# Kernel tuning notes

Measured on AMD Instinct MI355X. Metric: run time of the kernel, lower is better.

Reference implementation:

```python
import jax, jax.numpy as jnp
import numpy as np

B, SQ, SK, D, H = 2, 2048, 2048, 1024, 16
DK = D // H


def setup_inputs() -> dict:
    key = jax.random.key(0)
    ks = jax.random.split(key, 16)
    s = 1.0 / np.sqrt(D)
    inp = {
        "query": jax.random.normal(ks[0], (B, SQ, D), jnp.float32),
        "key": jax.random.normal(ks[1], (B, SK, D), jnp.float32),
        "value": jax.random.normal(ks[2], (B, SK, D), jnp.float32),
        "R": jax.random.normal(ks[3], (B, SK, D), jnp.float32),
        "Wq": jax.random.normal(ks[4], (D, D), jnp.float32) * s,
        "bq": jnp.zeros((D,), jnp.float32),
        "Wv": jax.random.normal(ks[5], (D, D), jnp.float32) * s,
        "bv": jnp.zeros((D,), jnp.float32),
        "Wr": jax.random.normal(ks[6], (D, D), jnp.float32) * s,
        "br": jnp.zeros((D,), jnp.float32),
        "W_h": jax.random.normal(ks[7], (H, DK, DK), jnp.float32) * (1.0 / np.sqrt(DK)),
        "Wo": jax.random.normal(ks[8], (D, D), jnp.float32) * s,
        "bo": jnp.zeros((D,), jnp.float32),
    }
    return inp


def _forward(query, key, value, R, Wq, bq, Wv, bv, Wr, br, W_h, Wo, bo):
    scale = 1.0 / np.sqrt(DK)
    # projections (torch Linear: x @ W.T + b)
    Q = (query @ Wq.T + bq).reshape(B, SQ, H, DK).transpose(0, 2, 1, 3)   # (B,H,SQ,DK)
    V = (value @ Wv.T + bv).reshape(B, SK, H, DK).transpose(0, 2, 1, 3)   # (B,H,SK,DK)
    Rp = (R @ Wr.T + br).reshape(B, SK, H, DK).transpose(0, 2, 1, 3)      # (B,H,SK,DK)
    # torch einsum 'hnk,bhn->bhn' sums W_h over its last axis -> elementwise gate
    w_rowsum = W_h.sum(axis=-1)  # (H, DK)

    def step(h, r_t):
        h_new = jnp.tanh(h * w_rowsum + r_t)  # (B,H,DK)
        return h_new, h_new

    h0 = jnp.zeros((B, H, DK), Rp.dtype)
    Rt = Rp.transpose(2, 0, 1, 3)  # (SK,B,H,DK)
    _, Hs = jax.lax.scan(step, h0, Rt)
    Hst = Hs.transpose(1, 2, 0, 3)  # (B,H,SK,DK)

    scores = jnp.einsum('bhqd,bhkd->bhqk', Q, Hst) * scale
    attn = jax.nn.softmax(scores, axis=-1)
    out = jnp.einsum('bhqk,bhkd->bhqd', attn, V)
    out = out.transpose(0, 2, 1, 3).reshape(B, SQ, D)
    return out @ Wo.T + bo


def reference(query, key, value, R, Wq, bq, Wv, bv, Wr, br, W_h, Wo, bo):
    return _forward(query, key, value, R, Wq, bq, Wv, bv, Wr, br, W_h, Wo, bo)
```

## Files before the change

kernel.cpp:

```cpp
#include <hip/hip_runtime.h>
#include <stdint.h>

typedef unsigned short u16;
typedef __attribute__((ext_vector_type(8))) _Float16 h8;
typedef __attribute__((ext_vector_type(2))) __fp16 hp2;
typedef __attribute__((ext_vector_type(4))) float f4;

#define B_ 2
#define SQ_ 2048
#define SK_ 2048
#define D_ 1024
#define H_ 16
#define DK_ 64

__device__ __forceinline__ u16 f2h(float f) {
  union { _Float16 h; u16 u; } v; v.h = (_Float16)f; return v.u;
}
__device__ __forceinline__ float h2f(u16 b) {
  union { u16 u; _Float16 h; } v; v.u = b; return (float)v.h;
}
__device__ __forceinline__ unsigned pkrtz(float a, float b) {
  union { hp2 h; unsigned u; } v; v.h = __builtin_amdgcn_cvt_pkrtz(a, b); return v.u;
}
__device__ __forceinline__ float fexp2(float x) {
  float r;
  asm("v_exp_f32 %0, %1" : "=v"(r) : "v"(x));
  return r;
}

typedef const void __attribute__((address_space(1)))* gas1;
typedef void __attribute__((address_space(3)))* las3;
__device__ __forceinline__ void gld16(const void* g, void* l) {
  __builtin_amdgcn_global_load_lds((gas1)g, (las3)l, 16, 0, 0);
}

__global__ void rma_cast(const float* __restrict__ xq, const float* __restrict__ xv,
                         const float* __restrict__ xr, const float* __restrict__ w0,
                         const float* __restrict__ w1, const float* __restrict__ w2,
                         const float* __restrict__ w3, u16* __restrict__ oq,
                         u16* __restrict__ ov, u16* __restrict__ orr,
                         u16* __restrict__ o0, u16* __restrict__ o1,
                         u16* __restrict__ o2, u16* __restrict__ o3) {
  const int z = blockIdx.z;
  if (z >= 3 && blockIdx.x >= 512) return;
  const float* src;
  u16* dst;
  switch (z) {
    case 0: src = xq; dst = oq; break;
    case 1: src = xv; dst = ov; break;
    case 2: src = xr; dst = orr; break;
    case 3: src = w0; dst = o0; break;
    case 4: src = w1; dst = o1; break;
    case 5: src = w2; dst = o2; break;
    default: src = w3; dst = o3; break;
  }
  int i = (blockIdx.x * 256 + threadIdx.x) * 8;
  float4 a = *(const float4*)(src + i);
  float4 b = *(const float4*)(src + i + 4);
  alignas(16) u16 t[8] = {f2h(a.x), f2h(a.y), f2h(a.z), f2h(a.w),
                          f2h(b.x), f2h(b.y), f2h(b.z), f2h(b.w)};
  *(int4*)(dst + i) = *(int4*)t;
}

__device__ __forceinline__ void gemm_mainloop(
    const u16* __restrict__ A, const u16* __restrict__ Bw, int K,
    u16* As, u16* Bs, int m0, int n0, f4 (&acc)[4][4]) {
  const int tid = threadIdx.x;
  const int w = tid >> 6, lane = tid & 63;
  const int quad = lane >> 4, ln = lane & 15;
  const int wm = (w >> 1) * 64, wn = (w & 1) * 64;
  const int c0 = tid, c1 = tid + 256;
  const u16* a0 = A + (size_t)(m0 + (c0 >> 2)) * K + (c0 & 3) * 8;
  const u16* a1 = A + (size_t)(m0 + (c1 >> 2)) * K + (c1 & 3) * 8;
  const u16* b0 = Bw + (size_t)(n0 + (c0 >> 2)) * K + (c0 & 3) * 8;
  const u16* b1 = Bw + (size_t)(n0 + (c1 >> 2)) * K + (c1 & 3) * 8;
  u16* As0 = As + (0 + w * 64) * 8;
  u16* As1 = As + (256 + w * 64) * 8;
  u16* Bs0 = Bs + (0 + w * 64) * 8;
  u16* Bs1 = Bs + (256 + w * 64) * 8;
  for (int kt = 0; kt < K; kt += 32) {
    gld16(a0 + kt, As0);
    gld16(a1 + kt, As1);
    gld16(b0 + kt, Bs0);
    gld16(b1 + kt, Bs1);
    __syncthreads();
    h8 af[4], bf[4];
#pragma unroll
    for (int i = 0; i < 4; i++)
      af[i] = *(const h8*)&As[(wm + i * 16 + ln) * 32 + quad * 8];
#pragma unroll
    for (int i = 0; i < 4; i++)
      bf[i] = *(const h8*)&Bs[(wn + i * 16 + ln) * 32 + quad * 8];
#pragma unroll
    for (int i = 0; i < 4; i++)
#pragma unroll
      for (int j = 0; j < 4; j++)
        acc[i][j] = __builtin_amdgcn_mfma_f32_16x16x32_f16(af[i], bf[j], acc[i][j], 0, 0, 0);
    __syncthreads();
  }
}

__device__ __forceinline__ void gemm_mainloop64(
    const u16* __restrict__ A, const u16* __restrict__ Bw, int K,
    u16* As, u16* Bs, int m0, int n0, f4 (&acc)[2][4]) {
  const int tid = threadIdx.x;
  const int w = tid >> 6, lane = tid & 63;
  const int quad = lane >> 4, ln = lane & 15;
  const int wm = (w >> 1) * 32, wn = (w & 1) * 64;
  const u16* a0 = A + (size_t)(m0 + (tid >> 2)) * K + (tid & 3) * 8;
  const u16* b0 = Bw + (size_t)(n0 + (tid >> 2)) * K + (tid & 3) * 8;
  const u16* b1 = Bw + (size_t)(n0 + ((tid + 256) >> 2)) * K + (tid & 3) * 8;
  u16* As0 = As + (w * 64) * 8;
  u16* Bs0 = Bs + (w * 64) * 8;
  u16* Bs1 = Bs + (256 + w * 64) * 8;
  for (int kt = 0; kt < K; kt += 32) {
    gld16(a0 + kt, As0);
    gld16(b0 + kt, Bs0);
    gld16(b1 + kt, Bs1);
    __syncthreads();
    h8 af[2], bf[4];
#pragma unroll
    for (int i = 0; i < 2; i++)
      af[i] = *(const h8*)&As[(wm + i * 16 + ln) * 32 + quad * 8];
#pragma unroll
    for (int j = 0; j < 4; j++)
      bf[j] = *(const h8*)&Bs[(wn + j * 16 + ln) * 32 + quad * 8];
#pragma unroll
    for (int i = 0; i < 2; i++)
#pragma unroll
      for (int j = 0; j < 4; j++)
        acc[i][j] = __builtin_amdgcn_mfma_f32_16x16x32_f16(af[i], bf[j], acc[i][j], 0, 0, 0);
    __syncthreads();
  }
}

__global__ __launch_bounds__(256, 2)
void rma_proj_gemm(const u16* __restrict__ Xq, const u16* __restrict__ Xv,
                   const u16* __restrict__ Xr, const u16* __restrict__ Wq,
                   const u16* __restrict__ Wv, const u16* __restrict__ Wr,
                   const float* __restrict__ bq, const float* __restrict__ bv,
                   const float* __restrict__ br, u16* __restrict__ Qb,
                   u16* __restrict__ Vt, float* __restrict__ Rp) {
  const int z = blockIdx.z;
  const u16* A = z == 0 ? Xq : (z == 1 ? Xv : Xr);
  const u16* Bw = z == 0 ? Wq : (z == 1 ? Wv : Wr);
  const float* bias = z == 0 ? bq : (z == 1 ? bv : br);
  __shared__ u16 As[128 * 32];
  __shared__ u16 Bs[128 * 32];
  const int m0 = blockIdx.x * 128, n0 = blockIdx.y * 128;
  f4 acc[4][4] = {};
  gemm_mainloop(A, Bw, D_, As, Bs, m0, n0, acc);
  const int tid = threadIdx.x;
  const int w = tid >> 6, lane = tid & 63;
  const int quad = lane >> 4, ln = lane & 15;
  const int wm = (w >> 1) * 64, wn = (w & 1) * 64;
#pragma unroll
  for (int i = 0; i < 4; i++)
#pragma unroll
    for (int j = 0; j < 4; j++) {
      const int colg = n0 + wn + j * 16 + ln;
      const float bb = bias[colg];
      const int h = colg >> 6, d = colg & 63;
      const int row4 = m0 + wm + i * 16 + quad * 4;
      const int b = row4 >> 11, s = row4 & 2047;
      if (z == 1) {
        uint2 pk;
        pk.x = pkrtz(acc[i][j][0] + bb, acc[i][j][1] + bb);
        pk.y = pkrtz(acc[i][j][2] + bb, acc[i][j][3] + bb);
        *(uint2*)&Vt[((size_t)((b * H_ + h) * DK_ + d)) * SK_ + s] = pk;
      } else {
#pragma unroll
        for (int r = 0; r < 4; r++) {
          const float v = acc[i][j][r] + bb;
          const size_t idx = ((size_t)(b * H_ + h) * SK_ + (s + r)) * DK_ + d;
          if (z == 2) Rp[idx] = v;
          else Qb[idx] = f2h(v);
        }
      }
    }
}

__global__ __launch_bounds__(256, 2)
void rma_final_gemm(const u16* __restrict__ Og, const u16* __restrict__ Wo,
                    const float* __restrict__ bo, float* __restrict__ out) {
  __shared__ u16 As[64 * 32];
  __shared__ u16 Bs[128 * 32];
  const int m0 = blockIdx.x * 64, n0 = blockIdx.y * 128;
  f4 acc[2][4] = {};
  gemm_mainloop64(Og, Wo, D_, As, Bs, m0, n0, acc);
  const int tid = threadIdx.x;
  const int w = tid >> 6, lane = tid & 63;
  const int quad = lane >> 4, ln = lane & 15;
  const int wm = (w >> 1) * 32, wn = (w & 1) * 64;
#pragma unroll
  for (int i = 0; i < 2; i++)
#pragma unroll
    for (int j = 0; j < 4; j++) {
      const int colg = n0 + wn + j * 16 + ln;
      const float bb = bo[colg];
#pragma unroll
      for (int r = 0; r < 4; r++) {
        const int rowg = m0 + wm + i * 16 + quad * 4 + r;
        out[(size_t)rowg * D_ + colg] = acc[i][j][r] + bb;
      }
    }
}

#define RB_ 32
__global__ __launch_bounds__(64)
void rma_recurrence(const float* __restrict__ Rp, const float* __restrict__ Wh,
                    u16* __restrict__ Hst) {
  const int bh = blockIdx.x;
  const int d = threadIdx.x;
  const int h = bh & 15;
  const float* wr = Wh + (h * 64 + d) * 64;
  float ws = 0.f;
#pragma unroll
  for (int k = 0; k < 64; k += 4) {
    float4 wv = *(const float4*)(wr + k);
    ws += (wv.x + wv.y) + (wv.z + wv.w);
  }
  const float C2 = 2.885390081777927f;
  const float wc = ws * C2;
  const size_t base = (size_t)bh * (SK_ * DK_) + d;
  const float* r = Rp + base;
  u16* o = Hst + base;
  float cur[RB_], nxt[RB_];
#pragma unroll
  for (int j = 0; j < RB_; j++) cur[j] = r[(size_t)j * DK_];
  float hs = 0.f;
  for (int t0 = 0; t0 < SK_; t0 += RB_) {
    const int tn = (t0 + RB_ < SK_) ? (t0 + RB_) : t0;
#pragma unroll
    for (int j = 0; j < RB_; j++) nxt[j] = r[(size_t)(tn + j) * DK_];
#pragma unroll
    for (int j = 0; j < RB_; j++) {
      const float cc = cur[j] * C2;
      float x = __builtin_fmaf(hs, wc, cc);
      float e = fexp2(x);
      float inv = __builtin_amdgcn_rcpf(e + 1.0f);
      hs = __builtin_fmaf(-2.0f, inv, 1.0f);
      o[(size_t)(t0 + j) * DK_] = f2h(hs);
    }
#pragma unroll
    for (int j = 0; j < RB_; j++) cur[j] = nxt[j];
  }
}

#define FXM_ 12.0f
__global__ __launch_bounds__(256, 2)
void rma_flash(const u16* __restrict__ Qb, const u16* __restrict__ Hst,
               const u16* __restrict__ Vt, u16* __restrict__ Og) {
  __shared__ u16 Kt[64 * 72];
  __shared__ u16 Vts[64 * 72];
  __shared__ u16 Ps[4][32 * 72];
  const int tid = threadIdx.x;
  const int w = tid >> 6, lane = tid & 63;
  const int quad = lane >> 4, ln = lane & 15;
  const int bh = blockIdx.y;
  const int q0 = blockIdx.x * 128 + w * 32;
  const float scale2 = 0.18033688011112042f;
  const u16* Qg = Qb + (size_t)bh * SQ_ * DK_;
  const u16* Kg = Hst + (size_t)bh * SK_ * DK_;
  const u16* Vg = Vt + (size_t)bh * DK_ * SK_;
  u16* Pw = Ps[w];
  h8 qf[2][2];
#pragma unroll
  for (int qt = 0; qt < 2; qt++)
#pragma unroll
    for (int c = 0; c < 2; c++)
      qf[qt][c] = *(const h8*)&Qg[(size_t)(q0 + qt * 16 + ln) * DK_ + c * 32 + quad * 8];
  f4 o[4][2] = {};
  float l[2] = {0.f, 0.f};

  const int c0 = tid, c1 = tid + 256;
  const int r0 = c0 >> 3, o0 = (c0 & 7) * 8;
  const int r1 = c1 >> 3, o1 = (c1 & 7) * 8;
  const u16* kg0 = Kg + (size_t)r0 * DK_ + o0;
  const u16* kg1 = Kg + (size_t)r1 * DK_ + o1;
  const u16* vg0 = Vg + (size_t)r0 * SK_ + o0;
  const u16* vg1 = Vg + (size_t)r1 * SK_ + o1;
  u16* kl0 = &Kt[r0 * 72 + o0];
  u16* kl1 = &Kt[r1 * 72 + o1];
  u16* vl0 = &Vts[r0 * 72 + o0];
  u16* vl1 = &Vts[r1 * 72 + o1];

  int4 ks0 = *(const int4*)(kg0);
  int4 ks1 = *(const int4*)(kg1);
  int4 vs0 = *(const int4*)(vg0);
  int4 vs1 = *(const int4*)(vg1);

  for (int kt = 0; kt < SK_; kt += 64) {
    __syncthreads();
    *(int4*)kl0 = ks0;
    *(int4*)kl1 = ks1;
    *(int4*)vl0 = vs0;
    *(int4*)vl1 = vs1;
    __syncthreads();
    h8 kf[4][2], vf[4][2];
#pragma unroll
    for (int m = 0; m < 4; m++) {
      kf[m][0] = *(const h8*)&Kt[(m * 16 + ln) * 72 + quad * 8];
      kf[m][1] = *(const h8*)&Kt[(m * 16 + ln) * 72 + 32 + quad * 8];
    }
#pragma unroll
    for (int dt = 0; dt < 4; dt++) {
      vf[dt][0] = *(const h8*)&Vts[(dt * 16 + ln) * 72 + quad * 8];
      vf[dt][1] = *(const h8*)&Vts[(dt * 16 + ln) * 72 + 32 + quad * 8];
    }
    const int ktn = (kt + 64 < SK_) ? kt + 64 : 0;
    ks0 = *(const int4*)(kg0 + (size_t)ktn * DK_);
    ks1 = *(const int4*)(kg1 + (size_t)ktn * DK_);
    vs0 = *(const int4*)(vg0 + ktn);
    vs1 = *(const int4*)(vg1 + ktn);
    f4 st[4][2];
#pragma unroll
    for (int m = 0; m < 4; m++)
#pragma unroll
      for (int qt = 0; qt < 2; qt++) {
        f4 t = {0.f, 0.f, 0.f, 0.f};
        t = __builtin_amdgcn_mfma_f32_16x16x32_f16(kf[m][0], qf[qt][0], t, 0, 0, 0);
        t = __builtin_amdgcn_mfma_f32_16x16x32_f16(kf[m][1], qf[qt][1], t, 0, 0, 0);
        st[m][qt] = t;
      }
#pragma unroll
    for (int qt = 0; qt < 2; qt++)
#pragma unroll
      for (int m = 0; m < 4; m++) {
        const float p0 = fexp2(__builtin_fmaf(st[m][qt][0], scale2, -FXM_));
        const float p1 = fexp2(__builtin_fmaf(st[m][qt][1], scale2, -FXM_));
        const float p2 = fexp2(__builtin_fmaf(st[m][qt][2], scale2, -FXM_));
        const float p3 = fexp2(__builtin_fmaf(st[m][qt][3], scale2, -FXM_));
        l[qt] += (p0 + p1) + (p2 + p3);
        uint2 pk;
        pk.x = pkrtz(p0, p1);
        pk.y = pkrtz(p2, p3);
        *(uint2*)&Pw[(qt * 16 + ln) * 72 + m * 16 + quad * 4] = pk;
      }
    asm volatile("" ::: "memory");
#pragma unroll
    for (int c = 0; c < 2; c++) {
      h8 pb0 = *(const h8*)&Pw[(0 + ln) * 72 + c * 32 + quad * 8];
      h8 pb1 = *(const h8*)&Pw[(16 + ln) * 72 + c * 32 + quad * 8];
#pragma unroll
      for (int dt = 0; dt < 4; dt++) {
        o[dt][0] = __builtin_amdgcn_mfma_f32_16x16x32_f16(vf[dt][c], pb0, o[dt][0], 0, 0, 0);
        o[dt][1] = __builtin_amdgcn_mfma_f32_16x16x32_f16(vf[dt][c], pb1, o[dt][1], 0, 0, 0);
      }
    }
  }
  const int b = bh >> 4, h = bh & 15;
#pragma unroll
  for (int qt = 0; qt < 2; qt++) {
    float lq = l[qt];
    lq += __shfl_xor(lq, 16);
    lq += __shfl_xor(lq, 32);
    const float linv = __builtin_amdgcn_rcpf(lq);
    const int q = q0 + qt * 16 + ln;
#pragma unroll
    for (int dt = 0; dt < 4; dt++) {
      uint2 pk;
      pk.x = pkrtz(o[dt][qt][0] * linv, o[dt][qt][1] * linv);
      pk.y = pkrtz(o[dt][qt][2] * linv, o[dt][qt][3] * linv);
      *(uint2*)&Og[((size_t)b * SQ_ + q) * D_ + h * DK_ + dt * 16 + quad * 4] = pk;
    }
  }
}

extern "C" void kernel_launch(void* const* d_in, const int* in_sizes, int n_in,
                              void* d_out, int out_size, void* d_ws, size_t ws_size,
                              hipStream_t stream) {
  const float* query = (const float*)d_in[0];
  const float* value = (const float*)d_in[2];
  const float* R = (const float*)d_in[3];
  const float* Wq = (const float*)d_in[4];
  const float* bq = (const float*)d_in[5];
  const float* Wv = (const float*)d_in[6];
  const float* bv = (const float*)d_in[7];
  const float* Wr = (const float*)d_in[8];
  const float* br = (const float*)d_in[9];
  const float* W_h = (const float*)d_in[10];
  const float* Wo = (const float*)d_in[11];
  const float* bo = (const float*)d_in[12];
  float* out = (float*)d_out;

  char* ws = (char*)d_ws;
  const size_t MB = 1 << 20;
  u16* Xq = (u16*)(ws + 0 * MB);
  u16* Xv = (u16*)(ws + 8 * MB);
  u16* Xr = (u16*)(ws + 16 * MB);
  u16* Wqb = (u16*)(ws + 24 * MB);
  u16* Wvb = (u16*)(ws + 26 * MB);
  u16* Wrb = (u16*)(ws + 28 * MB);
  u16* Wob = (u16*)(ws + 30 * MB);
  u16* Qb = (u16*)(ws + 32 * MB);
  u16* Vt = (u16*)(ws + 40 * MB);
  float* Rp = (float*)(ws + 48 * MB);
  u16* Hs = (u16*)(ws + 64 * MB);
  u16* Og = (u16*)(ws + 72 * MB);

  rma_cast<<<dim3(2048, 1, 7), 256, 0, stream>>>(query, value, R, Wq, Wv, Wr, Wo,
                                                 Xq, Xv, Xr, Wqb, Wvb, Wrb, Wob);
  rma_proj_gemm<<<dim3(32, 8, 3), 256, 0, stream>>>(Xq, Xv, Xr, Wqb, Wvb, Wrb,
                                                    bq, bv, br, Qb, Vt, Rp);
  rma_recurrence<<<dim3(32), 64, 0, stream>>>(Rp, W_h, Hs);
  rma_flash<<<dim3(16, 32), 256, 0, stream>>>(Qb, Hs, Vt, Og);
  rma_final_gemm<<<dim3(64, 8), 256, 0, stream>>>(Og, Wob, bo, out);
}
```

Measured before the change: 300.5 us.

## Overlap serial recurrence with Q/V projection GEMMs in one launch

Splits the projection GEMM so the R projection runs first, then launches a combined kernel in which the first 8 blocks run the serial tanh recurrence (four heads per block) while the remaining blocks compute the Q and V projections. This hides the long, latency-bound recurrence behind GEMM work instead of running it alone on 32 tiny blocks. The recurrence is also rewritten to carry exp(2x) instead of h, which shortens the dependent chain per step. It adds a branch-divergent mixed kernel whose recurrence blocks hold GEMM-sized shared memory and launch bounds.

```diff
diff --git a/kernel.cpp b/kernel.cpp
--- a/kernel.cpp
+++ b/kernel.cpp
@@ -135,22 +135,93 @@
 }
 
 __global__ __launch_bounds__(256, 2)
-void rma_proj_gemm(const u16* __restrict__ Xq, const u16* __restrict__ Xv,
-                   const u16* __restrict__ Xr, const u16* __restrict__ Wq,
-                   const u16* __restrict__ Wv, const u16* __restrict__ Wr,
-                   const float* __restrict__ bq, const float* __restrict__ bv,
-                   const float* __restrict__ br, u16* __restrict__ Qb,
-                   u16* __restrict__ Vt, float* __restrict__ Rp) {
-  const int z = blockIdx.z;
-  const u16* A = z == 0 ? Xq : (z == 1 ? Xv : Xr);
-  const u16* Bw = z == 0 ? Wq : (z == 1 ? Wv : Wr);
-  const float* bias = z == 0 ? bq : (z == 1 ? bv : br);
+void rma_projr(const u16* __restrict__ Xr, const u16* __restrict__ Wr,
+               const float* __restrict__ br, float* __restrict__ Rp) {
   __shared__ u16 As[128 * 32];
   __shared__ u16 Bs[128 * 32];
   const int m0 = blockIdx.x * 128, n0 = blockIdx.y * 128;
   f4 acc[4][4] = {};
+  gemm_mainloop(Xr, Wr, D_, As, Bs, m0, n0, acc);
+  const int tid = threadIdx.x;
+  const int w = tid >> 6, lane = tid & 63;
+  const int quad = lane >> 4, ln = lane & 15;
+  const int wm = (w >> 1) * 64, wn = (w & 1) * 64;
+#pragma unroll
+  for (int i = 0; i < 4; i++)
+#pragma unroll
+    for (int j = 0; j < 4; j++) {
+      const int colg = n0 + wn + j * 16 + ln;
+      const float bb = br[colg];
+      const int h = colg >> 6, d = colg & 63;
+      const int row4 = m0 + wm + i * 16 + quad * 4;
+      const int b = row4 >> 11, s = row4 & 2047;
+#pragma unroll
+      for (int r = 0; r < 4; r++)
+        Rp[((size_t)(b * H_ + h) * SK_ + (s + r)) * DK_ + d] = acc[i][j][r] + bb;
+    }
+}
+
+#define RB_ 32
+__global__ __launch_bounds__(256, 2)
+void rma_projqv_rec(const u16* __restrict__ Xq, const u16* __restrict__ Xv,
+                    const u16* __restrict__ Wq, const u16* __restrict__ Wv,
+                    const float* __restrict__ bq, const float* __restrict__ bv,
+                    u16* __restrict__ Qb, u16* __restrict__ Vt,
+                    const float* __restrict__ Rp, const float* __restrict__ Wh,
+                    u16* __restrict__ Hst) {
+  __shared__ u16 As[128 * 32];
+  __shared__ u16 Bs[128 * 32];
+  const int bid = blockIdx.x;
+  const int tid = threadIdx.x;
+  if (bid < 8) {
+    const int w = tid >> 6, d = tid & 63;
+    const int bh = bid * 4 + w;
+    const int h = bh & 15;
+    const float* wr = Wh + (h * 64 + d) * 64;
+    float ws = 0.f;
+#pragma unroll
+    for (int k = 0; k < 64; k += 4) {
+      float4 wv = *(const float4*)(wr + k);
+      ws += (wv.x + wv.y) + (wv.z + wv.w);
+    }
+    const float C2 = 2.885390081777927f;
+    const float cw = C2 * ws;
+    const float wc2 = -2.0f * cw;
+    const size_t base = (size_t)bh * (SK_ * DK_) + d;
+    const float* r = Rp + base;
+    u16* o = Hst + base;
+    float cur[RB_], nxt[RB_];
+#pragma unroll
+    for (int j = 0; j < RB_; j++) cur[j] = r[(size_t)j * DK_];
+    float u = 1.0f;
+    for (int t0 = 0; t0 < SK_; t0 += RB_) {
+      const int tn = (t0 + RB_ < SK_) ? (t0 + RB_) : t0;
+#pragma unroll
+      for (int j = 0; j < RB_; j++) nxt[j] = r[(size_t)(tn + j) * DK_];
+#pragma unroll
+      for (int j = 0; j < RB_; j++) {
+        const float bt = __builtin_fmaf(C2, cur[j], cw);
+        const float inv = __builtin_amdgcn_rcpf(u + 1.0f);
+        u = fexp2(__builtin_fmaf(wc2, inv, bt));
+        if (t0 + j > 0)
+          o[(size_t)(t0 + j - 1) * DK_] = f2h(__builtin_fmaf(-2.0f, inv, 1.0f));
+      }
+#pragma unroll
+      for (int j = 0; j < RB_; j++) cur[j] = nxt[j];
+    }
+    const float invf = __builtin_amdgcn_rcpf(u + 1.0f);
+    o[(size_t)(SK_ - 1) * DK_] = f2h(__builtin_fmaf(-2.0f, invf, 1.0f));
+    return;
+  }
+  const int rb = bid - 8;
+  const int z = rb >> 8;
+  const int rem = rb & 255;
+  const int m0 = (rem & 31) * 128, n0 = (rem >> 5) * 128;
+  const u16* A = z == 0 ? Xq : Xv;
+  const u16* Bw = z == 0 ? Wq : Wv;
+  const float* bias = z == 0 ? bq : bv;
+  f4 acc[4][4] = {};
   gemm_mainloop(A, Bw, D_, As, Bs, m0, n0, acc);
-  const int tid = threadIdx.x;
   const int w = tid >> 6, lane = tid & 63;
   const int quad = lane >> 4, ln = lane & 15;
   const int wm = (w >> 1) * 64, wn = (w & 1) * 64;
@@ -170,12 +241,8 @@
         *(uint2*)&Vt[((size_t)((b * H_ + h) * DK_ + d)) * SK_ + s] = pk;
       } else {
 #pragma unroll
-        for (int r = 0; r < 4; r++) {
-          const float v = acc[i][j][r] + bb;
-          const size_t idx = ((size_t)(b * H_ + h) * SK_ + (s + r)) * DK_ + d;
-          if (z == 2) Rp[idx] = v;
-          else Qb[idx] = f2h(v);
-        }
+        for (int r = 0; r < 4; r++)
+          Qb[((size_t)(b * H_ + h) * SK_ + (s + r)) * DK_ + d] = f2h(acc[i][j][r] + bb);
       }
     }
 }
@@ -204,47 +271,6 @@
         out[(size_t)rowg * D_ + colg] = acc[i][j][r] + bb;
       }
     }
-}
-
-#define RB_ 32
-__global__ __launch_bounds__(64)
-void rma_recurrence(const float* __restrict__ Rp, const float* __restrict__ Wh,
-                    u16* __restrict__ Hst) {
-  const int bh = blockIdx.x;
-  const int d = threadIdx.x;
-  const int h = bh & 15;
-  const float* wr = Wh + (h * 64 + d) * 64;
-  float ws = 0.f;
-#pragma unroll
-  for (int k = 0; k < 64; k += 4) {
-    float4 wv = *(const float4*)(wr + k);
-    ws += (wv.x + wv.y) + (wv.z + wv.w);
-  }
-  const float C2 = 2.885390081777927f;
-  const float wc = ws * C2;
-  const size_t base = (size_t)bh * (SK_ * DK_) + d;
-  const float* r = Rp + base;
-  u16* o = Hst + base;
-  float cur[RB_], nxt[RB_];
-#pragma unroll
-  for (int j = 0; j < RB_; j++) cur[j] = r[(size_t)j * DK_];
-  float hs = 0.f;
-  for (int t0 = 0; t0 < SK_; t0 += RB_) {
-    const int tn = (t0 + RB_ < SK_) ? (t0 + RB_) : t0;
-#pragma unroll
-    for (int j = 0; j < RB_; j++) nxt[j] = r[(size_t)(tn + j) * DK_];
-#pragma unroll
-    for (int j = 0; j < RB_; j++) {
-      const float cc = cur[j] * C2;
-      float x = __builtin_fmaf(hs, wc, cc);
-      float e = fexp2(x);
-      float inv = __builtin_amdgcn_rcpf(e + 1.0f);
-      hs = __builtin_fmaf(-2.0f, inv, 1.0f);
-      o[(size_t)(t0 + j) * DK_] = f2h(hs);
-    }
-#pragma unroll
-    for (int j = 0; j < RB_; j++) cur[j] = nxt[j];
-  }
 }
 
 #define FXM_ 12.0f
@@ -401,9 +427,9 @@
 
   rma_cast<<<dim3(2048, 1, 7), 256, 0, stream>>>(query, value, R, Wq, Wv, Wr, Wo,
                                                  Xq, Xv, Xr, Wqb, Wvb, Wrb, Wob);
-  rma_proj_gemm<<<dim3(32, 8, 3), 256, 0, stream>>>(Xq, Xv, Xr, Wqb, Wvb, Wrb,
-                                                    bq, bv, br, Qb, Vt, Rp);
-  rma_recurrence<<<dim3(32), 64, 0, stream>>>(Rp, W_h, Hs);
+  rma_projr<<<dim3(32, 8), 256, 0, stream>>>(Xr, Wrb, br, Rp);
+  rma_projqv_rec<<<dim3(520), 256, 0, stream>>>(Xq, Xv, Wqb, Wvb, bq, bv,
+                                                Qb, Vt, Rp, W_h, Hs);
   rma_flash<<<dim3(16, 32), 256, 0, stream>>>(Qb, Hs, Vt, Og);
   rma_final_gemm<<<dim3(64, 8), 256, 0, stream>>>(Og, Wob, bo, out);
 }
```

Measured after the change: 301.3 us. About the same (+0.2%).
